# Kernel optimization log

Hardware: AMD Instinct MI355X
Metric: run time of the kernel (lower is better)

## Reference

```python
import jax, jax.numpy as jnp
import numpy as np

DEPTH, EMBED, HEADS, FF = 4, 512, 8, 2048
POS_SCALE, POS_WEIGHT = 0.1, 1.0
EPS = 1e-5  # torch LayerNorm default


def setup_inputs() -> dict:
    key = jax.random.key(0)
    ks = jax.random.split(key, 6)
    B, L = 8, 1024
    s = 0.02
    x = jax.random.normal(ks[0], (B, L, EMBED), jnp.float32)
    Wqkv = jax.random.normal(ks[1], (DEPTH, 3 * EMBED, EMBED), jnp.float32) * s
    bqkv = jnp.zeros((DEPTH, 3 * EMBED), jnp.float32)
    W1 = jax.random.normal(ks[2], (DEPTH, FF, EMBED), jnp.float32) * s
    b1 = jnp.zeros((DEPTH, FF), jnp.float32)
    W2 = jax.random.normal(ks[3], (DEPTH, EMBED, FF), jnp.float32) * s
    b2 = jnp.zeros((DEPTH, EMBED), jnp.float32)
    g = jnp.ones((DEPTH, EMBED), jnp.float32)
    bt = jnp.zeros((DEPTH, EMBED), jnp.float32)
    return {"input": x, "Wqkv": Wqkv, "bqkv": bqkv, "W1": W1, "b1": b1,
            "W2": W2, "b2": b2, "g1": g, "bt1": bt, "g2": g, "bt2": bt,
            "g3": g, "bt3": bt}


def _ln(x, g, b):
    m = x.mean(-1, keepdims=True)
    v = ((x - m) ** 2).mean(-1, keepdims=True)
    return (x - m) * jax.lax.rsqrt(v + EPS) * g + b


def reference(input, Wqkv, bqkv, W1, b1, W2, b2, g1, bt1, g2, bt2, g3, bt3):
    x = input
    B, L, E = x.shape
    hd = E // HEADS
    pos_idx = jnp.arange(L)
    # additive relative-position bias: exp(-|i-j| * scale) * weight
    pos = jnp.exp(-jnp.abs(pos_idx[:, None] - pos_idx[None, :]).astype(x.dtype) * POS_SCALE) * POS_WEIGHT
    triu = jnp.triu(jnp.ones((L, L), dtype=bool), 1)
    inv_sqrt_hd = jnp.asarray(1.0 / np.sqrt(hd), x.dtype)
    for d in range(DEPTH):
        # --- RelativeMultiheadAttention self-attn block ---
        qkv = jnp.einsum('ble,fe->blf', x, Wqkv[d]) + bqkv[d]
        q = qkv[..., :E].reshape(B, L, HEADS, hd).transpose(0, 2, 1, 3)
        k = qkv[..., E:2 * E].reshape(B, L, HEADS, hd).transpose(0, 2, 1, 3)
        logits = jnp.einsum('bhqd,bhkd->bhqk', q, k) * inv_sqrt_hd
        # nn.MultiheadAttention returns head-AVERAGED softmax weights
        A = jax.nn.softmax(logits, axis=-1).mean(axis=1)  # [B,L,L]
        # torch: attn_logits[triu(attn_logits,1).to(bool)] = -inf (nonzero strict upper)
        A = jnp.where(triu & (A != 0), -jnp.inf, A)
        W = jax.nn.softmax(A + pos[None], axis=-1)
        sa = jnp.einsum('bqk,bke->bqe', W, x)  # value is RAW x (no v-proj/out-proj)
        x = _ln(x + sa, g1[d], bt1[d])
        # --- NoopAttention cross-attn block contributes zeros ---
        x = _ln(x, g2[d], bt2[d])
        # --- FFN block (relu activation, post-norm) ---
        h = jax.nn.relu(jnp.einsum('ble,fe->blf', x, W1[d]) + b1[d])
        ff = jnp.einsum('blf,ef->ble', h, W2[d]) + b2[d]
        x = _ln(x + ff, g3[d], bt3[d])
    return x
```

## Files before the change

### kernel.cpp

```cpp
#include <hip/hip_runtime.h>

#define NB 8
#define SEQ 1024
#define EMB 512
#define FFD 2048
#define NROWS (NB*SEQ)
#define LNEPS 1e-5f

typedef __bf16 bf16x8 __attribute__((ext_vector_type(8)));
typedef float f32x4 __attribute__((ext_vector_type(4)));

__device__ __forceinline__ unsigned short f2bf(float f){
  unsigned u = __builtin_bit_cast(unsigned, f);
  u += 0x7fffu + ((u>>16)&1u);
  return (unsigned short)(u>>16);
}
__device__ __forceinline__ bf16x8 ld_bf8(const unsigned short* p){
  return *(const bf16x8*)p;
}
__device__ __forceinline__ void async_copy16(const void* g, void* l){
  __builtin_amdgcn_global_load_lds((const __attribute__((address_space(1))) unsigned int*)g,
                                   (__attribute__((address_space(3))) unsigned int*)l,
                                   16, 0, 0);
}

__device__ __forceinline__ float2 block_sum2(float a,float b){
  #pragma unroll
  for(int k=32;k>=1;k>>=1){ a += __shfl_xor(a,k,64); b += __shfl_xor(b,k,64); }
  __shared__ float sa[4], sb[4];
  int w = threadIdx.x>>6;
  __syncthreads();
  if((threadIdx.x&63)==0){ sa[w]=a; sb[w]=b; }
  __syncthreads();
  return make_float2(sa[0]+sa[1]+sa[2]+sa[3], sb[0]+sb[1]+sb[2]+sb[3]);
}

template<bool OUTBF16, bool RELU, bool BIAS, bool CAUSAL, int NT>
__global__ __launch_bounds__(256) void gemm_bf16(
    const unsigned short* __restrict__ Ag, const unsigned short* __restrict__ Bg,
    const float* __restrict__ bias, void* __restrict__ Cg,
    int K, int lda, int ldb, int ldc,
    long long strA, long long strB, long long strC)
{
  constexpr int NJ = NT/32;
  __shared__ unsigned short As[128*32];
  __shared__ unsigned short Bs[NT*32];
  const unsigned short* Ab = Ag + blockIdx.z*strA;
  const unsigned short* Bb = Bg + blockIdx.z*strB;
  const int m0 = blockIdx.y*128, n0 = blockIdx.x*NT;
  const int t = threadIdx.x;
  const int lane = t & 63, w = t >> 6;
  const int wy = w >> 1, wx = w & 1;
  const int q = lane >> 4, c = lane & 15;
  f32x4 acc[4][NJ] = {};
  const int kend = CAUSAL ? (m0 + 128) : K;
  const int srow = t >> 2;
  const int sk = (t & 3) * 8;
  const int gk = ((t & 3) ^ ((t >> 3) & 3)) * 8;
  const int rs = (q ^ ((c >> 1) & 3)) * 8;
  for(int k0 = 0; k0 < kend; k0 += 32){
    async_copy16(Ab + (long long)(m0 + srow)*lda + k0 + gk,      As + srow*32 + sk);
    async_copy16(Ab + (long long)(m0 + srow + 64)*lda + k0 + gk, As + (srow+64)*32 + sk);
    async_copy16(Bb + (long long)(n0 + srow)*ldb + k0 + gk,      Bs + srow*32 + sk);
    if(NT == 128)
      async_copy16(Bb + (long long)(n0 + srow + 64)*ldb + k0 + gk, Bs + (srow+64)*32 + sk);
    __syncthreads();
    bf16x8 af[4], bfr[NJ];
    #pragma unroll
    for(int fi=0; fi<4; fi++) af[fi]  = ld_bf8(As + (wy*64 + fi*16 + c)*32 + rs);
    #pragma unroll
    for(int fj=0; fj<NJ; fj++) bfr[fj] = ld_bf8(Bs + (wx*(NT/2) + fj*16 + c)*32 + rs);
    #pragma unroll
    for(int fi=0; fi<4; fi++)
      #pragma unroll
      for(int fj=0; fj<NJ; fj++)
        acc[fi][fj] = __builtin_amdgcn_mfma_f32_16x16x32_bf16(af[fi], bfr[fj], acc[fi][fj], 0,0,0);
    __syncthreads();
  }
  #pragma unroll
  for(int fi=0; fi<4; fi++){
    #pragma unroll
    for(int fj=0; fj<NJ; fj++){
      const int row = m0 + wy*64 + fi*16 + q*4;
      const int col = n0 + wx*(NT/2) + fj*16 + c;
      const float bv = (BIAS && blockIdx.z==0) ? bias[col] : 0.f;
      #pragma unroll
      for(int r=0; r<4; r++){
        float v = acc[fi][fj][r] + bv;
        if(RELU) v = fmaxf(v, 0.f);
        long long off = blockIdx.z*strC + (long long)(row+r)*ldc + col;
        if(OUTBF16) ((unsigned short*)Cg)[off] = f2bf(v);
        else        ((float*)Cg)[off] = v;
      }
    }
  }
}

__global__ __launch_bounds__(256) void qk_dsum(
    const unsigned short* __restrict__ qkv, float* __restrict__ dsum)
{
  __shared__ unsigned short As[128*32];
  __shared__ unsigned short Bs[128*32];
  const int bh = blockIdx.z, b = bh >> 3, h = bh & 7;
  const int i0 = blockIdx.y*128, j0 = blockIdx.x*128;
  const unsigned short* Ab = qkv + (long long)b*SEQ*1024 + h*64;
  const unsigned short* Bb = qkv + (long long)b*SEQ*1024 + 512 + h*64;
  const int t = threadIdx.x, lane = t & 63, w = t >> 6;
  const int wy = w >> 1, wx = w & 1, q = lane >> 4, c = lane & 15;
  f32x4 acc[4][4] = {};
  const int srow = t >> 2;
  const int sk = (t & 3) * 8;
  const int gk = ((t & 3) ^ ((t >> 3) & 3)) * 8;
  const int rs = (q ^ ((c >> 1) & 3)) * 8;
  #pragma unroll
  for(int k0 = 0; k0 < 64; k0 += 32){
    async_copy16(Ab + (long long)(i0 + srow)*1024 + k0 + gk,      As + srow*32 + sk);
    async_copy16(Ab + (long long)(i0 + srow + 64)*1024 + k0 + gk, As + (srow+64)*32 + sk);
    async_copy16(Bb + (long long)(j0 + srow)*1024 + k0 + gk,      Bs + srow*32 + sk);
    async_copy16(Bb + (long long)(j0 + srow + 64)*1024 + k0 + gk, Bs + (srow+64)*32 + sk);
    __syncthreads();
    bf16x8 af[4], bfr[4];
    #pragma unroll
    for(int fi=0; fi<4; fi++) af[fi]  = ld_bf8(As + (wy*64 + fi*16 + c)*32 + rs);
    #pragma unroll
    for(int fj=0; fj<4; fj++) bfr[fj] = ld_bf8(Bs + (wx*64 + fj*16 + c)*32 + rs);
    #pragma unroll
    for(int fi=0; fi<4; fi++)
      #pragma unroll
      for(int fj=0; fj<4; fj++)
        acc[fi][fj] = __builtin_amdgcn_mfma_f32_16x16x32_bf16(af[fi], bfr[fj], acc[fi][fj], 0,0,0);
    __syncthreads();
  }
  #pragma unroll
  for(int fi=0; fi<4; fi++){
    #pragma unroll
    for(int r=0; r<4; r++){
      float s = 0.f;
      #pragma unroll
      for(int fj=0; fj<4; fj++) s += __expf(acc[fi][fj][r]*0.125f);
      s += __shfl_xor(s,1,64); s += __shfl_xor(s,2,64);
      s += __shfl_xor(s,4,64); s += __shfl_xor(s,8,64);
      if(c == 0)
        atomicAdd(&dsum[(long long)bh*SEQ + i0 + wy*64 + fi*16 + q*4 + r], s);
    }
  }
}

__global__ __launch_bounds__(256) void attn_w(
    const unsigned short* __restrict__ qkv, const float* __restrict__ dsum,
    unsigned short* __restrict__ Wm, float* __restrict__ Dsum2)
{
  __shared__ unsigned short As[64*32];
  __shared__ unsigned short Bs[64*32];
  __shared__ float inv8[8][64];
  const int b = blockIdx.y;
  int x = blockIdx.x;
  int it = 0;
  while((it+1)*(it+2)/2 <= x) ++it;
  const int jt = x - it*(it+1)/2;
  const int i0 = it*64, j0 = jt*64;
  const int t = threadIdx.x, lane = t & 63, w = t >> 6;
  const int q = lane >> 4, c = lane & 15;
  for(int u = t; u < 512; u += 256){
    int h = u >> 6, r = u & 63;
    inv8[h][r] = 1.f/(8.f*dsum[((long long)(b*8 + h))*SEQ + i0 + r]);
  }
  const unsigned short* Qb = qkv + (long long)b*SEQ*1024;
  const int srow = t >> 2;
  const int sk = (t & 3) * 8;
  const int gk = ((t & 3) ^ ((t >> 3) & 3)) * 8;
  const int rs = (q ^ ((c >> 1) & 3)) * 8;
  f32x4 at[4] = {};
  for(int h = 0; h < 8; h++){
    f32x4 l[4] = {};
    #pragma unroll
    for(int k0 = 0; k0 < 64; k0 += 32){
      __syncthreads();
      async_copy16(Qb + (long long)(i0 + srow)*1024 + h*64 + k0 + gk,       As + srow*32 + sk);
      async_copy16(Qb + (long long)(j0 + srow)*1024 + 512 + h*64 + k0 + gk, Bs + srow*32 + sk);
      __syncthreads();
      bf16x8 af = ld_bf8(As + (w*16 + c)*32 + rs);
      bf16x8 bfr[4];
      #pragma unroll
      for(int fj=0; fj<4; fj++) bfr[fj] = ld_bf8(Bs + (fj*16 + c)*32 + rs);
      #pragma unroll
      for(int fj=0; fj<4; fj++)
        l[fj] = __builtin_amdgcn_mfma_f32_16x16x32_bf16(af, bfr[fj], l[fj], 0,0,0);
    }
    #pragma unroll
    for(int r=0; r<4; r++){
      float iv = inv8[h][w*16 + q*4 + r];
      #pragma unroll
      for(int fj=0; fj<4; fj++)
        at[fj][r] += __expf(l[fj][r]*0.125f)*iv;
    }
  }
  float Dacc[4] = {};
  #pragma unroll
  for(int fj=0; fj<4; fj++){
    #pragma unroll
    for(int r=0; r<4; r++){
      const int i = i0 + w*16 + q*4 + r;
      const int j = j0 + fj*16 + c;
      float wv = 0.f;
      if(j <= i) wv = __expf(at[fj][r] + __expf((float)(j - i)*0.1f));
      Wm[((long long)(b*SEQ + i))*SEQ + j] = f2bf(wv);
      Dacc[r] += wv;
    }
  }
  #pragma unroll
  for(int r=0; r<4; r++){
    Dacc[r] += __shfl_xor(Dacc[r],1,64); Dacc[r] += __shfl_xor(Dacc[r],2,64);
    Dacc[r] += __shfl_xor(Dacc[r],4,64); Dacc[r] += __shfl_xor(Dacc[r],8,64);
    if(c == 0)
      atomicAdd(&Dsum2[(long long)b*SEQ + i0 + w*16 + q*4 + r], Dacc[r]);
  }
}

__global__ __launch_bounds__(256) void transpose_bf16(
    const unsigned short* __restrict__ src, unsigned short* __restrict__ dst)
{
  __shared__ unsigned short tile[64*65];
  const int bx = blockIdx.x;
  const int by = blockIdx.y;
  const int t = threadIdx.x;
  #pragma unroll
  for(int p=0; p<2; p++){
    int idx = t + p*256;
    int r = idx >> 3, cc = (idx & 7)*8;
    alignas(16) unsigned short e[8];
    *(uint4*)e = *(const uint4*)(src + (long long)(by*64 + r)*512 + bx*64 + cc);
    #pragma unroll
    for(int u=0; u<8; u++) tile[r*65 + cc + u] = e[u];
  }
  __syncthreads();
  #pragma unroll
  for(int p=0; p<2; p++){
    int idx = t + p*256;
    int r2 = idx >> 3, c2 = (idx & 7)*8;
    alignas(16) unsigned short e[8];
    #pragma unroll
    for(int u=0; u<8; u++) e[u] = tile[(c2+u)*65 + r2];
    *(uint4*)(dst + (long long)(bx*64 + r2)*8192 + by*64 + c2) = *(const uint4*)e;
  }
}

__global__ __launch_bounds__(256) void residual_ln2(
    const float* __restrict__ X, const float* __restrict__ SA,
    const float* __restrict__ Dsum2,
    const float* __restrict__ g1, const float* __restrict__ b1,
    const float* __restrict__ g2, const float* __restrict__ b2,
    float* __restrict__ XO, unsigned short* __restrict__ Xb)
{
  const long long row = blockIdx.x;
  const int t = threadIdx.x;
  const float s = 1.f/Dsum2[row];
  float v0 = X[row*EMB + t]       + SA[row*EMB + t]*s;
  float v1 = X[row*EMB + t + 256] + SA[row*EMB + t + 256]*s;
  float2 ss = block_sum2(v0+v1, v0*v0+v1*v1);
  float mean = ss.x*(1.f/EMB);
  float var  = ss.y*(1.f/EMB) - mean*mean;
  float rstd = rsqrtf(var + LNEPS);
  float y0 = (v0-mean)*rstd*g1[t]     + b1[t];
  float y1 = (v1-mean)*rstd*g1[t+256] + b1[t+256];
  ss = block_sum2(y0+y1, y0*y0+y1*y1);
  mean = ss.x*(1.f/EMB);
  var  = ss.y*(1.f/EMB) - mean*mean;
  rstd = rsqrtf(var + LNEPS);
  float o0 = (y0-mean)*rstd*g2[t]     + b2[t];
  float o1 = (y1-mean)*rstd*g2[t+256] + b2[t+256];
  XO[row*EMB + t] = o0;       XO[row*EMB + t + 256] = o1;
  Xb[row*EMB + t] = f2bf(o0); Xb[row*EMB + t + 256] = f2bf(o1);
}

__global__ __launch_bounds__(256) void residual_ln(
    const float* __restrict__ X, const float* __restrict__ R1,
    const float* __restrict__ R2,
    const float* __restrict__ g, const float* __restrict__ b,
    float* __restrict__ XO, unsigned short* __restrict__ Xb)
{
  const long long row = blockIdx.x;
  const int t = threadIdx.x;
  float v0 = X[row*EMB + t]       + R1[row*EMB + t]       + R2[row*EMB + t];
  float v1 = X[row*EMB + t + 256] + R1[row*EMB + t + 256] + R2[row*EMB + t + 256];
  float2 ss = block_sum2(v0+v1, v0*v0+v1*v1);
  float mean = ss.x*(1.f/EMB);
  float var  = ss.y*(1.f/EMB) - mean*mean;
  float rstd = rsqrtf(var + LNEPS);
  float o0 = (v0-mean)*rstd*g[t]     + b[t];
  float o1 = (v1-mean)*rstd*g[t+256] + b[t+256];
  XO[row*EMB + t] = o0;       XO[row*EMB + t + 256] = o1;
  Xb[row*EMB + t] = f2bf(o0); Xb[row*EMB + t + 256] = f2bf(o1);
}

__global__ __launch_bounds__(256) void init_x(
    const float* __restrict__ in, float* __restrict__ XO,
    unsigned short* __restrict__ Xb)
{
  const long long row = blockIdx.x;
  const int t = threadIdx.x;
  float v0 = in[row*EMB + t];
  float v1 = in[row*EMB + t + 256];
  XO[row*EMB + t] = v0;       XO[row*EMB + t + 256] = v1;
  Xb[row*EMB + t] = f2bf(v0); Xb[row*EMB + t + 256] = f2bf(v1);
}

__global__ __launch_bounds__(256) void cvt_bf16(
    const float* __restrict__ src, unsigned short* __restrict__ dst, long long n)
{
  long long i = ((long long)blockIdx.x*256 + threadIdx.x)*4;
  if(i < n){
    float4 v = *(const float4*)(src + i);
    ushort4 o = make_ushort4(f2bf(v.x), f2bf(v.y), f2bf(v.z), f2bf(v.w));
    *(ushort4*)(dst + i) = o;
  }
}

__global__ __launch_bounds__(256) void cvt_qkv(
    const float* __restrict__ src, unsigned short* __restrict__ dst)
{
  long long i = ((long long)blockIdx.x*256 + threadIdx.x)*4;
  int layer = (int)(i >> 19);
  long long within = i & ((1LL<<19)-1);
  float4 v = *(const float4*)(src + (long long)layer*1536*512 + within);
  ushort4 o = make_ushort4(f2bf(v.x), f2bf(v.y), f2bf(v.z), f2bf(v.w));
  *(ushort4*)(dst + i) = o;
}

extern "C" void kernel_launch(void* const* d_in, const int* in_sizes, int n_in,
                              void* d_out, int out_size, void* d_ws, size_t ws_size,
                              hipStream_t stream)
{
  const float* x_in = (const float*)d_in[0];
  const float* Wqkv = (const float*)d_in[1];
  const float* bqkv = (const float*)d_in[2];
  const float* W1   = (const float*)d_in[3];
  const float* b1   = (const float*)d_in[4];
  const float* W2   = (const float*)d_in[5];
  const float* b2   = (const float*)d_in[6];
  const float* g1   = (const float*)d_in[7];
  const float* bt1  = (const float*)d_in[8];
  const float* g2   = (const float*)d_in[9];
  const float* bt2  = (const float*)d_in[10];
  const float* g3   = (const float*)d_in[11];
  const float* bt3  = (const float*)d_in[12];

  float* X = (float*)d_out;

  char* ws = (char*)d_ws;
  unsigned short* qkv    = (unsigned short*)(ws);
  unsigned short* hbuf   = (unsigned short*)(ws + ((size_t)16<<20));
  unsigned short* Wm     = (unsigned short*)(ws + ((size_t)48<<20));
  float*          tmp    = (float*)         (ws + ((size_t)64<<20));
  float*          tmp2   = (float*)         (ws + ((size_t)80<<20));
  unsigned short* Xb     = (unsigned short*)(ws + ((size_t)96<<20));
  unsigned short* XT     = (unsigned short*)(ws + ((size_t)104<<20));
  unsigned short* Wqkvb  = (unsigned short*)(ws + ((size_t)112<<20));
  unsigned short* W1b    = (unsigned short*)(ws + ((size_t)118<<20));
  unsigned short* W2b    = (unsigned short*)(ws + ((size_t)126<<20));
  float*          dsum   = (float*)         (ws + ((size_t)134<<20));
  float*          Dsum2  = (float*)         (ws + ((size_t)134<<20) + (256<<10));

  cvt_qkv<<<2048, 256, 0, stream>>>(Wqkv, Wqkvb);
  cvt_bf16<<<4096, 256, 0, stream>>>(W1, W1b, (long long)4*FFD*EMB);
  cvt_bf16<<<4096, 256, 0, stream>>>(W2, W2b, (long long)4*EMB*FFD);
  init_x<<<NROWS, 256, 0, stream>>>(x_in, X, Xb);
  transpose_bf16<<<dim3(8,128), 256, 0, stream>>>(Xb, XT);

  for(int d=0; d<4; d++){
    hipMemsetAsync(dsum, 0, (256<<10) + (32<<10), stream);

    gemm_bf16<true,false,true,false,128><<<dim3(8, 64, 1), 256, 0, stream>>>(
        Xb, Wqkvb + (size_t)d*1024*EMB, bqkv + (size_t)d*1536, qkv,
        EMB, EMB, EMB, 1024, 0, 0, 0);

    qk_dsum<<<dim3(8, 8, 64), 256, 0, stream>>>(qkv, dsum);

    attn_w<<<dim3(136, NB), 256, 0, stream>>>(qkv, dsum, Wm, Dsum2);

    gemm_bf16<false,false,false,true,64><<<dim3(8, 8, NB), 256, 0, stream>>>(
        Wm, XT, nullptr, tmp,
        SEQ, SEQ, NROWS, EMB,
        (long long)SEQ*SEQ, 1024, (long long)SEQ*EMB);

    residual_ln2<<<NROWS, 256, 0, stream>>>(X, tmp, Dsum2,
        g1 + d*EMB, bt1 + d*EMB, g2 + d*EMB, bt2 + d*EMB, X, Xb);

    gemm_bf16<true,true,true,false,128><<<dim3(16, 64, 1), 256, 0, stream>>>(
        Xb, W1b + (size_t)d*FFD*EMB, b1 + (size_t)d*FFD, hbuf,
        EMB, EMB, EMB, FFD, 0, 0, 0);

    gemm_bf16<false,false,true,false,128><<<dim3(4, 64, 2), 256, 0, stream>>>(
        hbuf, W2b + (size_t)d*EMB*FFD, b2 + (size_t)d*EMB, tmp,
        1024, FFD, FFD, EMB,
        1024, 1024, (long long)NROWS*EMB);

    residual_ln<<<NROWS, 256, 0, stream>>>(X, tmp, tmp2,
        g3 + d*EMB, bt3 + d*EMB, X, Xb);
    transpose_bf16<<<dim3(8,128), 256, 0, stream>>>(Xb, XT);
  }
}
```

Before: 997.3 us.

## Add double-buffered 256x128 tile GEMM for QKV and FFN projections

Introduces a new GEMM kernel with 512 threads, 256x128 output tiles and double-buffered LDS staging through async global-to-LDS copies, so the next K-slice loads while MFMAs run on the current one. It replaces the 128-row tile GEMM for the QKV projection and both FFN matmuls. Larger tiles raise operand reuse per LDS load, and double buffering aims to hide load latency. The cost is higher register and LDS use per block and fewer blocks for the smaller QKV grid, which may lower occupancy and load balance.

```diff
diff --git a/kernel.cpp b/kernel.cpp
--- a/kernel.cpp
+++ b/kernel.cpp
@@ -33,6 +33,70 @@
   if((threadIdx.x&63)==0){ sa[w]=a; sb[w]=b; }
   __syncthreads();
   return make_float2(sa[0]+sa[1]+sa[2]+sa[3], sb[0]+sb[1]+sb[2]+sb[3]);
+}
+
+template<bool OUTBF16, bool RELU, bool BIAS>
+__global__ __launch_bounds__(512,2) void gemm_big(
+    const unsigned short* __restrict__ Ag, const unsigned short* __restrict__ Bg,
+    const float* __restrict__ bias, void* __restrict__ Cg,
+    int K, int lda, int ldb, int ldc,
+    long long strA, long long strB, long long strC)
+{
+  __shared__ unsigned short As[2][256*32];
+  __shared__ unsigned short Bs[2][128*32];
+  const unsigned short* Ab = Ag + blockIdx.z*strA;
+  const unsigned short* Bb = Bg + blockIdx.z*strB;
+  const int m0 = blockIdx.y*256, n0 = blockIdx.x*128;
+  const int t = threadIdx.x;
+  const int lane = t & 63, w = t >> 6;
+  const int wy = w >> 1, wx = w & 1;
+  const int q = lane >> 4, c = lane & 15;
+  const int rA = t >> 2;
+  const int gk = (((t & 3) ^ ((t >> 3) & 3)))*8;
+  const int sO = t*8;
+  const int rs = (q ^ ((c >> 1) & 3)) * 8;
+  f32x4 acc[4][4] = {};
+
+#define STAGE(bi, kk) do { \
+    async_copy16(Ab + (long long)(m0 + rA)*lda + (kk) + gk,       &As[bi][sO]); \
+    async_copy16(Ab + (long long)(m0 + 128 + rA)*lda + (kk) + gk, &As[bi][4096 + sO]); \
+    async_copy16(Bb + (long long)(n0 + rA)*ldb + (kk) + gk,       &Bs[bi][sO]); \
+  } while(0)
+
+  STAGE(0, 0);
+  int buf = 0;
+  for(int k0 = 0; k0 < K; k0 += 32, buf ^= 1){
+    __syncthreads();
+    if(k0 + 32 < K) STAGE(buf^1, k0 + 32);
+    bf16x8 af[4], bfr[4];
+    #pragma unroll
+    for(int fi=0; fi<4; fi++) af[fi]  = ld_bf8(&As[buf][(wy*64 + fi*16 + c)*32 + rs]);
+    #pragma unroll
+    for(int fj=0; fj<4; fj++) bfr[fj] = ld_bf8(&Bs[buf][(wx*64 + fj*16 + c)*32 + rs]);
+    #pragma unroll
+    for(int fi=0; fi<4; fi++)
+      #pragma unroll
+      for(int fj=0; fj<4; fj++)
+        acc[fi][fj] = __builtin_amdgcn_mfma_f32_16x16x32_bf16(af[fi], bfr[fj], acc[fi][fj], 0,0,0);
+  }
+#undef STAGE
+  #pragma unroll
+  for(int fi=0; fi<4; fi++){
+    #pragma unroll
+    for(int fj=0; fj<4; fj++){
+      const int row = m0 + wy*64 + fi*16 + q*4;
+      const int col = n0 + wx*64 + fj*16 + c;
+      const float bv = (BIAS && blockIdx.z==0) ? bias[col] : 0.f;
+      #pragma unroll
+      for(int r=0; r<4; r++){
+        float v = acc[fi][fj][r] + bv;
+        if(RELU) v = fmaxf(v, 0.f);
+        long long off = blockIdx.z*strC + (long long)(row+r)*ldc + col;
+        if(OUTBF16) ((unsigned short*)Cg)[off] = f2bf(v);
+        else        ((float*)Cg)[off] = v;
+      }
+    }
+  }
 }
 
 template<bool OUTBF16, bool RELU, bool BIAS, bool CAUSAL, int NT>
@@ -370,7 +434,7 @@
   for(int d=0; d<4; d++){
     hipMemsetAsync(dsum, 0, (256<<10) + (32<<10), stream);
 
-    gemm_bf16<true,false,true,false,128><<<dim3(8, 64, 1), 256, 0, stream>>>(
+    gemm_big<true,false,true><<<dim3(8, 32, 1), 512, 0, stream>>>(
         Xb, Wqkvb + (size_t)d*1024*EMB, bqkv + (size_t)d*1536, qkv,
         EMB, EMB, EMB, 1024, 0, 0, 0);
 
@@ -386,11 +450,11 @@
     residual_ln2<<<NROWS, 256, 0, stream>>>(X, tmp, Dsum2,
         g1 + d*EMB, bt1 + d*EMB, g2 + d*EMB, bt2 + d*EMB, X, Xb);
 
-    gemm_bf16<true,true,true,false,128><<<dim3(16, 64, 1), 256, 0, stream>>>(
+    gemm_big<true,true,true><<<dim3(16, 32, 1), 512, 0, stream>>>(
         Xb, W1b + (size_t)d*FFD*EMB, b1 + (size_t)d*FFD, hbuf,
         EMB, EMB, EMB, FFD, 0, 0, 0);
 
-    gemm_bf16<false,false,true,false,128><<<dim3(4, 64, 2), 256, 0, stream>>>(
+    gemm_big<false,false,true><<<dim3(4, 32, 2), 512, 0, stream>>>(
         hbuf, W2b + (size_t)d*EMB*FFD, b2 + (size_t)d*EMB, tmp,
         1024, FFD, FFD, EMB,
         1024, 1024, (long long)NROWS*EMB);
```

New measurement: 968.0 us. 1.03x faster.
